# Optimization experiments

Measured on AMD Instinct MI355X. Metric: run time of the kernel, lower is better.

The kernel has to match this reference:

```python
import jax, jax.numpy as jnp
import numpy as np

B, H, W = 4, 64, 1024
h, w = 32, 512
K = 16
C = 64
EPS = 1e-5


def setup_inputs() -> dict:
    key = jax.random.key(0)
    ks = jax.random.split(key, 8)
    n_sampled = h * w
    xyz_proj = jax.random.normal(ks[0], (B, H, W, 3), dtype=jnp.float32)
    points_proj = jax.random.normal(ks[1], (B, H, W, C), dtype=jnp.float32)
    xyz_sampled_proj = jax.random.normal(ks[2], (B, h, w, 3), dtype=jnp.float32)
    # Precomputed neighbor selection (stand-in for fused_conv_random_k, which is
    # a non-differentiable custom CUDA op producing detached indices + mask).
    neighbor_idx = jax.random.randint(ks[3], (B, n_sampled * K), 0, H * W, dtype=jnp.int32)
    valid_mask = (jax.random.uniform(ks[4], (B, n_sampled, K, 1)) > 0.1).astype(jnp.float32)
    # 1x1 conv MLP params (torch Conv2d weight (out,in,1,1) stored here as (in,out))
    def mk(k, cin, cout):
        kw, = jax.random.split(k, 1)
        wgt = jax.random.normal(kw, (cin, cout), dtype=jnp.float32) * (1.0 / np.sqrt(cin))
        return wgt
    w0 = mk(ks[5], 3 + C, 64)
    w1 = mk(ks[6], 64, 64)
    w2 = mk(ks[7], 64, 128)
    z = lambda c: jnp.zeros((c,), jnp.float32)
    o = lambda c: jnp.ones((c,), jnp.float32)
    return dict(
        xyz_proj=xyz_proj, points_proj=points_proj, xyz_sampled_proj=xyz_sampled_proj,
        neighbor_idx=neighbor_idx, valid_mask=valid_mask,
        w0=w0, b0=z(64), g0=o(64), be0=z(64), m0=z(64), v0=o(64),
        w1=w1, b1=z(64), g1=o(64), be1=z(64), m1=z(64), v1=o(64),
        w2=w2, b2=z(128), g2=o(128), be2=z(128), m2=z(128), v2=o(128),
    )


def _conv_bn_relu(x, wgt, b, g, be, m, v):
    # 1x1 conv == matmul over channel dim; BN in eval mode with running stats.
    y = jnp.einsum('bnkc,co->bnko', x, wgt) + b
    y = g * (y - m) * jax.lax.rsqrt(v + EPS) + be
    return jax.nn.relu(y)


def reference(xyz_proj, points_proj, xyz_sampled_proj, neighbor_idx, valid_mask,
              w0, b0, g0, be0, m0, v0,
              w1, b1, g1, be1, m1, v1,
              w2, b2, g2, be2, m2, v2):
    Bc = xyz_proj.shape[0]
    Cc = points_proj.shape[3]
    hh, ww = xyz_sampled_proj.shape[1], xyz_sampled_proj.shape[2]
    n_sampled = hh * ww
    xyz_bn3 = xyz_proj.reshape(Bc, -1, 3)          # (B, H*W, 3)
    points_bnc = points_proj.reshape(Bc, -1, Cc)   # (B, H*W, C)
    idx = neighbor_idx[..., None]                  # (B, n*K, 1)
    new_xyz_group = jnp.take_along_axis(xyz_bn3, idx, axis=1).reshape(Bc, n_sampled, K, 3)
    new_points_group = jnp.take_along_axis(points_bnc, idx, axis=1).reshape(Bc, n_sampled, K, Cc)
    new_xyz_group = new_xyz_group * valid_mask
    new_points_group = new_points_group * valid_mask
    new_xyz = xyz_sampled_proj.reshape(Bc, n_sampled, 1, 3)
    xyz_diff = new_xyz_group - new_xyz             # broadcast over K
    feat = jnp.concatenate([xyz_diff, new_points_group], axis=-1)  # (B, n, K, 3+C)
    feat = _conv_bn_relu(feat, w0, b0, g0, be0, m0, v0)
    feat = _conv_bn_relu(feat, w1, b1, g1, be1, m1, v1)
    feat = _conv_bn_relu(feat, w2, b2, g2, be2, m2, v2)
    points_down_sample = jnp.max(feat, axis=2)     # (B, n, 128) max-pool over K
    points_down_sample_proj = points_down_sample.reshape(Bc, hh, ww, -1)
    return points_down_sample, points_down_sample_proj
```

## Files before the change

### kernel.cpp

```cpp
#include <hip/hip_runtime.h>
#include <hip/hip_bf16.h>


#define HW_      65536
#define NPT_     16384
#define OUTHALF_ 8388608
#define F0S_     104
#define XS_      72
#define EPS_     1e-5f

typedef _Float16 h8    __attribute__((ext_vector_type(8)));
typedef float    f32x4 __attribute__((ext_vector_type(4)));
typedef unsigned short u16x8 __attribute__((ext_vector_type(8)));

__device__ __forceinline__ float bf2f(unsigned short u) {
    union { unsigned int i; float f; } x; x.i = ((unsigned int)u) << 16; return x.f;
}
__device__ __forceinline__ unsigned short f2bf(float f) {
    union { float f; unsigned int i; } x; x.f = f;
    unsigned int r = x.i + 0x7fffu + ((x.i >> 16) & 1u);
    return (unsigned short)(r >> 16);
}

template<bool F32>
__device__ __forceinline__ float ldp(const void* p, int i) {
    if (F32) return ((const float*)p)[i];
    return bf2f(((const unsigned short*)p)[i]);
}

template<bool F32>
__global__ __launch_bounds__(256, 2) void pnsa_kernel(
    const void* __restrict__ xyz,
    const void* __restrict__ pts,
    const void* __restrict__ xyzs,
    const int*  __restrict__ nidx,
    const void* __restrict__ vmask,
    const void* __restrict__ w0, const void* __restrict__ b0,
    const void* __restrict__ g0, const void* __restrict__ be0,
    const void* __restrict__ m0, const void* __restrict__ v0,
    const void* __restrict__ w1, const void* __restrict__ b1,
    const void* __restrict__ g1, const void* __restrict__ be1,
    const void* __restrict__ m1, const void* __restrict__ v1,
    const void* __restrict__ w2, const void* __restrict__ b2,
    const void* __restrict__ g2, const void* __restrict__ be2,
    const void* __restrict__ m2, const void* __restrict__ v2,
    void*       __restrict__ out)
{
    const unsigned int probe = *(const unsigned int*)v0;
    const bool isf32 = (probe == 0x3F800000u);
    if (isf32 != F32) return;

    __shared__ __align__(16) unsigned short ldsF0[4][16 * F0S_];
    __shared__ __align__(16) unsigned short ldsX1[4][16 * XS_];
    __shared__ __align__(16) unsigned short ldsX2[4][16 * XS_];

    const int tid  = threadIdx.x;
    const int wave = tid >> 6;
    const int lane = tid & 63;
    const int l15  = lane & 15;
    const int quad = lane >> 4;

    unsigned short* F0 = &ldsF0[wave][0];
    unsigned short* X1 = &ldsX1[wave][0];
    unsigned short* X2 = &ldsX2[wave][0];

    for (int i = lane; i < 16 * F0S_; i += 64) F0[i] = 0;

    h8    b0f[4][3], b1f[4][2], b2f[8][2];
    float t0r[4], t1r[4], t2r[8];

#pragma unroll
    for (int nt = 0; nt < 4; ++nt) {
        const int ch = nt * 16 + l15;
        const float s = ldp<F32>(g0, ch) * rsqrtf(ldp<F32>(v0, ch) + EPS_);
        t0r[nt] = (ldp<F32>(b0, ch) - ldp<F32>(m0, ch)) * s + ldp<F32>(be0, ch);
#pragma unroll
        for (int kk = 0; kk < 3; ++kk) {
            h8 f;
#pragma unroll
            for (int j = 0; j < 8; ++j) {
                const int k = kk * 32 + quad * 8 + j;
                float wv = 0.f;
                if (k < 64)      wv = ldp<F32>(w0, (3 + k) * 64 + ch);
                else if (k < 67) wv = ldp<F32>(w0, (k - 64) * 64 + ch);
                f[j] = (_Float16)(wv * s);
            }
            b0f[nt][kk] = f;
        }
    }
#pragma unroll
    for (int nt = 0; nt < 4; ++nt) {
        const int ch = nt * 16 + l15;
        const float s = ldp<F32>(g1, ch) * rsqrtf(ldp<F32>(v1, ch) + EPS_);
        t1r[nt] = (ldp<F32>(b1, ch) - ldp<F32>(m1, ch)) * s + ldp<F32>(be1, ch);
#pragma unroll
        for (int kk = 0; kk < 2; ++kk) {
            h8 f;
#pragma unroll
            for (int j = 0; j < 8; ++j)
                f[j] = (_Float16)(ldp<F32>(w1, (kk * 32 + quad * 8 + j) * 64 + ch) * s);
            b1f[nt][kk] = f;
        }
    }
#pragma unroll
    for (int nt = 0; nt < 8; ++nt) {
        const int ch = nt * 16 + l15;
        const float s = ldp<F32>(g2, ch) * rsqrtf(ldp<F32>(v2, ch) + EPS_);
        t2r[nt] = (ldp<F32>(b2, ch) - ldp<F32>(m2, ch)) * s + ldp<F32>(be2, ch);
#pragma unroll
        for (int kk = 0; kk < 2; ++kk) {
            h8 f;
#pragma unroll
            for (int j = 0; j < 8; ++j)
                f[j] = (_Float16)(ldp<F32>(w2, (kk * 32 + quad * 8 + j) * 128 + ch) * s);
            b2f[nt][kk] = f;
        }
    }

    const int kn  = lane >> 2;
    const int sub = lane & 3;

    for (int grp = blockIdx.x; grp < NPT_; grp += gridDim.x) {
        const int p  = (grp << 2) + wave;
        const int b  = p >> 14;
        const int np = p & (NPT_ - 1);

        const int   nb = nidx[((size_t)b << 18) + ((size_t)np << 4) + kn];
        const float mk = ldp<F32>(vmask, (p << 4) + kn);
        const size_t rowidx = (size_t)((b << 16) + nb);

        h8 lo, hi;
        if (F32) {
            const float* prow = (const float*)pts + (rowidx << 6) + sub * 16;
#pragma unroll
            for (int q = 0; q < 2; ++q) {
                f32x4 v = *(const f32x4*)(prow + q * 4);
#pragma unroll
                for (int j = 0; j < 4; ++j) lo[q * 4 + j] = (_Float16)v[j];
            }
#pragma unroll
            for (int q = 0; q < 2; ++q) {
                f32x4 v = *(const f32x4*)(prow + 8 + q * 4);
#pragma unroll
                for (int j = 0; j < 4; ++j) hi[q * 4 + j] = (_Float16)v[j];
            }
        } else {
            const unsigned short* prow = (const unsigned short*)pts + (rowidx << 6) + sub * 16;
            u16x8 p0 = *(const u16x8*)(prow);
            u16x8 p1 = *(const u16x8*)(prow + 8);
#pragma unroll
            for (int j = 0; j < 8; ++j) { lo[j] = (_Float16)bf2f(p0[j]); hi[j] = (_Float16)bf2f(p1[j]); }
        }
        if (mk == 0.0f) { lo = (h8)(_Float16)0.0f; hi = (h8)(_Float16)0.0f; }
        *(h8*)(F0 + kn * F0S_ + sub * 16)     = lo;
        *(h8*)(F0 + kn * F0S_ + sub * 16 + 8) = hi;

        if (sub == 0) {
            float xg0, xg1, xg2, xs0, xs1, xs2;
            if (F32) {
                const float* xg = (const float*)xyz  + rowidx * 3;
                const float* xs = (const float*)xyzs + (size_t)p * 3;
                xg0 = xg[0]; xg1 = xg[1]; xg2 = xg[2];
                xs0 = xs[0]; xs1 = xs[1]; xs2 = xs[2];
            } else {
                const unsigned short* xg = (const unsigned short*)xyz  + rowidx * 3;
                const unsigned short* xs = (const unsigned short*)xyzs + (size_t)p * 3;
                xg0 = bf2f(xg[0]); xg1 = bf2f(xg[1]); xg2 = bf2f(xg[2]);
                xs0 = bf2f(xs[0]); xs1 = bf2f(xs[1]); xs2 = bf2f(xs[2]);
            }
            _Float16 xd[4];
            xd[0] = (_Float16)(xg0 * mk - xs0);
            xd[1] = (_Float16)(xg1 * mk - xs1);
            xd[2] = (_Float16)(xg2 * mk - xs2);
            xd[3] = (_Float16)0.0f;
            *(unsigned long long*)(F0 + kn * F0S_ + 64) = *(unsigned long long*)xd;
        }

        h8 a[3];

#pragma unroll
        for (int kk = 0; kk < 3; ++kk)
            a[kk] = *(const h8*)(F0 + l15 * F0S_ + kk * 32 + quad * 8);
#pragma unroll
        for (int nt = 0; nt < 4; ++nt) {
            f32x4 acc = {0.f, 0.f, 0.f, 0.f};
#pragma unroll
            for (int kk = 0; kk < 3; ++kk)
                acc = __builtin_amdgcn_mfma_f32_16x16x32_f16(a[kk], b0f[nt][kk], acc, 0, 0, 0);
#pragma unroll
            for (int r = 0; r < 4; ++r) {
                const _Float16 hv = (_Float16)fmaxf(acc[r] + t0r[nt], 0.f);
                X1[(quad * 4 + r) * XS_ + nt * 16 + l15] = __builtin_bit_cast(unsigned short, hv);
            }
        }

#pragma unroll
        for (int kk = 0; kk < 2; ++kk)
            a[kk] = *(const h8*)(X1 + l15 * XS_ + kk * 32 + quad * 8);
#pragma unroll
        for (int nt = 0; nt < 4; ++nt) {
            f32x4 acc = {0.f, 0.f, 0.f, 0.f};
#pragma unroll
            for (int kk = 0; kk < 2; ++kk)
                acc = __builtin_amdgcn_mfma_f32_16x16x32_f16(a[kk], b1f[nt][kk], acc, 0, 0, 0);
#pragma unroll
            for (int r = 0; r < 4; ++r) {
                const _Float16 hv = (_Float16)fmaxf(acc[r] + t1r[nt], 0.f);
                X2[(quad * 4 + r) * XS_ + nt * 16 + l15] = __builtin_bit_cast(unsigned short, hv);
            }
        }

#pragma unroll
        for (int kk = 0; kk < 2; ++kk)
            a[kk] = *(const h8*)(X2 + l15 * XS_ + kk * 32 + quad * 8);
#pragma unroll
        for (int nt = 0; nt < 8; ++nt) {
            f32x4 acc = {0.f, 0.f, 0.f, 0.f};
#pragma unroll
            for (int kk = 0; kk < 2; ++kk)
                acc = __builtin_amdgcn_mfma_f32_16x16x32_f16(a[kk], b2f[nt][kk], acc, 0, 0, 0);
            float rm = 0.f;
#pragma unroll
            for (int r = 0; r < 4; ++r) rm = fmaxf(rm, acc[r] + t2r[nt]);
            rm = fmaxf(rm, __shfl_xor(rm, 16, 64));
            rm = fmaxf(rm, __shfl_xor(rm, 32, 64));
            if (quad == 0) {
                const int oidx = (p << 7) + nt * 16 + l15;
                if (F32) {
                    ((float*)out)[oidx]            = rm;
                    ((float*)out)[OUTHALF_ + oidx] = rm;
                } else {
                    const unsigned short ob = f2bf(rm);
                    ((unsigned short*)out)[oidx]            = ob;
                    ((unsigned short*)out)[OUTHALF_ + oidx] = ob;
                }
            }
        }
    }
}

extern "C" void kernel_launch(void* const* d_in, const int* in_sizes, int n_in,
                              void* d_out, int out_size, void* d_ws, size_t ws_size,
                              hipStream_t stream) {
    const void* xyz   = d_in[0];
    const void* pts   = d_in[1];
    const void* xyzs  = d_in[2];
    const int*  nidx  = (const int*)d_in[3];
    const void* vmask = d_in[4];
    const void *w0 = d_in[5],  *b0 = d_in[6],  *g0 = d_in[7],  *be0 = d_in[8],  *m0 = d_in[9],  *v0 = d_in[10];
    const void *w1 = d_in[11], *b1 = d_in[12], *g1 = d_in[13], *be1 = d_in[14], *m1 = d_in[15], *v1 = d_in[16];
    const void *w2 = d_in[17], *b2 = d_in[18], *g2 = d_in[19], *be2 = d_in[20], *m2 = d_in[21], *v2 = d_in[22];

    hipLaunchKernelGGL(pnsa_kernel<true>, dim3(1024), dim3(256), 0, stream,
                       xyz, pts, xyzs, nidx, vmask,
                       w0, b0, g0, be0, m0, v0,
                       w1, b1, g1, be1, m1, v1,
                       w2, b2, g2, be2, m2, v2, d_out);
    hipLaunchKernelGGL(pnsa_kernel<false>, dim3(1024), dim3(256), 0, stream,
                       xyz, pts, xyzs, nidx, vmask,
                       w0, b0, g0, be0, m0, v0,
                       w1, b1, g1, be1, m1, v1,
                       w2, b2, g2, be2, m2, v2, d_out);
}
```

Measured before the change: 264.9 us.

## Pre-convert points to fp16, load MFMA operands directly, prefetch next iteration

Drops the dual bf16/fp32 template launch and keeps only the fp32 path. When workspace allows, a separate kernel first converts points to fp16, halving the bytes of the random row gather. The gathered rows now load straight into MFMA A-fragments instead of going through an LDS staging buffer. A software pipeline prefetches neighbor indices and row data one or two iterations ahead, and outputs are written as coalesced full-wave stores. The cost is an extra full pass over the points tensor, which must be recovered by the cheaper gather.

Result: faster. 231.7 us (-12.5%).

```diff
diff --git a/kernel.cpp b/kernel.cpp
--- a/kernel.cpp
+++ b/kernel.cpp
@@ -1,56 +1,47 @@
 #include <hip/hip_runtime.h>
-#include <hip/hip_bf16.h>
 
 
 #define HW_      65536
 #define NPT_     16384
 #define OUTHALF_ 8388608
-#define F0S_     104
 #define XS_      72
 #define EPS_     1e-5f
+#define GRID_    1024
+#define NIT_     (NPT_ / GRID_)
 
 typedef _Float16 h8    __attribute__((ext_vector_type(8)));
 typedef float    f32x4 __attribute__((ext_vector_type(4)));
-typedef unsigned short u16x8 __attribute__((ext_vector_type(8)));
-
-__device__ __forceinline__ float bf2f(unsigned short u) {
-    union { unsigned int i; float f; } x; x.i = ((unsigned int)u) << 16; return x.f;
+
+__global__ __launch_bounds__(256) void cvt_pts_kernel(
+    const float* __restrict__ src, _Float16* __restrict__ dst)
+{
+    const size_t i = ((size_t)blockIdx.x * 256 + threadIdx.x) * 8;
+    f32x4 a = *(const f32x4*)(src + i);
+    f32x4 b = *(const f32x4*)(src + i + 4);
+    h8 o;
+#pragma unroll
+    for (int j = 0; j < 4; ++j) { o[j] = (_Float16)a[j]; o[4 + j] = (_Float16)b[j]; }
+    *(h8*)(dst + i) = o;
 }
-__device__ __forceinline__ unsigned short f2bf(float f) {
-    union { float f; unsigned int i; } x; x.f = f;
-    unsigned int r = x.i + 0x7fffu + ((x.i >> 16) & 1u);
-    return (unsigned short)(r >> 16);
-}
-
-template<bool F32>
-__device__ __forceinline__ float ldp(const void* p, int i) {
-    if (F32) return ((const float*)p)[i];
-    return bf2f(((const unsigned short*)p)[i]);
-}
-
-template<bool F32>
-__global__ __launch_bounds__(256, 2) void pnsa_kernel(
-    const void* __restrict__ xyz,
-    const void* __restrict__ pts,
-    const void* __restrict__ xyzs,
-    const int*  __restrict__ nidx,
-    const void* __restrict__ vmask,
-    const void* __restrict__ w0, const void* __restrict__ b0,
-    const void* __restrict__ g0, const void* __restrict__ be0,
-    const void* __restrict__ m0, const void* __restrict__ v0,
-    const void* __restrict__ w1, const void* __restrict__ b1,
-    const void* __restrict__ g1, const void* __restrict__ be1,
-    const void* __restrict__ m1, const void* __restrict__ v1,
-    const void* __restrict__ w2, const void* __restrict__ b2,
-    const void* __restrict__ g2, const void* __restrict__ be2,
-    const void* __restrict__ m2, const void* __restrict__ v2,
-    void*       __restrict__ out)
+
+template<bool PRE>
+__global__ __launch_bounds__(256, 2) void pnsa_main(
+    const float* __restrict__ xyz,
+    const void*  __restrict__ ptsv,
+    const float* __restrict__ xyzs,
+    const int*   __restrict__ nidx,
+    const float* __restrict__ vmask,
+    const float* __restrict__ w0, const float* __restrict__ b0,
+    const float* __restrict__ g0, const float* __restrict__ be0,
+    const float* __restrict__ m0, const float* __restrict__ v0,
+    const float* __restrict__ w1, const float* __restrict__ b1,
+    const float* __restrict__ g1, const float* __restrict__ be1,
+    const float* __restrict__ m1, const float* __restrict__ v1,
+    const float* __restrict__ w2, const float* __restrict__ b2,
+    const float* __restrict__ g2, const float* __restrict__ be2,
+    const float* __restrict__ m2, const float* __restrict__ v2,
+    float*       __restrict__ out)
 {
-    const unsigned int probe = *(const unsigned int*)v0;
-    const bool isf32 = (probe == 0x3F800000u);
-    if (isf32 != F32) return;
-
-    __shared__ __align__(16) unsigned short ldsF0[4][16 * F0S_];
     __shared__ __align__(16) unsigned short ldsX1[4][16 * XS_];
     __shared__ __align__(16) unsigned short ldsX2[4][16 * XS_];
 
@@ -60,20 +51,17 @@
     const int l15  = lane & 15;
     const int quad = lane >> 4;
 
-    unsigned short* F0 = &ldsF0[wave][0];
     unsigned short* X1 = &ldsX1[wave][0];
     unsigned short* X2 = &ldsX2[wave][0];
 
-    for (int i = lane; i < 16 * F0S_; i += 64) F0[i] = 0;
-
     h8    b0f[4][3], b1f[4][2], b2f[8][2];
     float t0r[4], t1r[4], t2r[8];
 
 #pragma unroll
     for (int nt = 0; nt < 4; ++nt) {
         const int ch = nt * 16 + l15;
-        const float s = ldp<F32>(g0, ch) * rsqrtf(ldp<F32>(v0, ch) + EPS_);
-        t0r[nt] = (ldp<F32>(b0, ch) - ldp<F32>(m0, ch)) * s + ldp<F32>(be0, ch);
+        const float s = g0[ch] * rsqrtf(v0[ch] + EPS_);
+        t0r[nt] = (b0[ch] - m0[ch]) * s + be0[ch];
 #pragma unroll
         for (int kk = 0; kk < 3; ++kk) {
             h8 f;
@@ -81,8 +69,8 @@
             for (int j = 0; j < 8; ++j) {
                 const int k = kk * 32 + quad * 8 + j;
                 float wv = 0.f;
-                if (k < 64)      wv = ldp<F32>(w0, (3 + k) * 64 + ch);
-                else if (k < 67) wv = ldp<F32>(w0, (k - 64) * 64 + ch);
+                if (k < 64)      wv = w0[(3 + k) * 64 + ch];
+                else if (k < 67) wv = w0[(k - 64) * 64 + ch];
                 f[j] = (_Float16)(wv * s);
             }
             b0f[nt][kk] = f;
@@ -91,102 +79,103 @@
 #pragma unroll
     for (int nt = 0; nt < 4; ++nt) {
         const int ch = nt * 16 + l15;
-        const float s = ldp<F32>(g1, ch) * rsqrtf(ldp<F32>(v1, ch) + EPS_);
-        t1r[nt] = (ldp<F32>(b1, ch) - ldp<F32>(m1, ch)) * s + ldp<F32>(be1, ch);
+        const float s = g1[ch] * rsqrtf(v1[ch] + EPS_);
+        t1r[nt] = (b1[ch] - m1[ch]) * s + be1[ch];
 #pragma unroll
         for (int kk = 0; kk < 2; ++kk) {
             h8 f;
 #pragma unroll
             for (int j = 0; j < 8; ++j)
-                f[j] = (_Float16)(ldp<F32>(w1, (kk * 32 + quad * 8 + j) * 64 + ch) * s);
+                f[j] = (_Float16)(w1[(kk * 32 + quad * 8 + j) * 64 + ch] * s);
             b1f[nt][kk] = f;
         }
     }
 #pragma unroll
     for (int nt = 0; nt < 8; ++nt) {
         const int ch = nt * 16 + l15;
-        const float s = ldp<F32>(g2, ch) * rsqrtf(ldp<F32>(v2, ch) + EPS_);
-        t2r[nt] = (ldp<F32>(b2, ch) - ldp<F32>(m2, ch)) * s + ldp<F32>(be2, ch);
+        const float s = g2[ch] * rsqrtf(v2[ch] + EPS_);
+        t2r[nt] = (b2[ch] - m2[ch]) * s + be2[ch];
 #pragma unroll
         for (int kk = 0; kk < 2; ++kk) {
             h8 f;
 #pragma unroll
             for (int j = 0; j < 8; ++j)
-                f[j] = (_Float16)(ldp<F32>(w2, (kk * 32 + quad * 8 + j) * 128 + ch) * s);
+                f[j] = (_Float16)(w2[(kk * 32 + quad * 8 + j) * 128 + ch] * s);
             b2f[nt][kk] = f;
         }
     }
 
-    const int kn  = lane >> 2;
-    const int sub = lane & 3;
-
-    for (int grp = blockIdx.x; grp < NPT_; grp += gridDim.x) {
-        const int p  = (grp << 2) + wave;
-        const int b  = p >> 14;
-        const int np = p & (NPT_ - 1);
-
-        const int   nb = nidx[((size_t)b << 18) + ((size_t)np << 4) + kn];
-        const float mk = ldp<F32>(vmask, (p << 4) + kn);
-        const size_t rowidx = (size_t)((b << 16) + nb);
-
-        h8 lo, hi;
-        if (F32) {
-            const float* prow = (const float*)pts + (rowidx << 6) + sub * 16;
-#pragma unroll
-            for (int q = 0; q < 2; ++q) {
-                f32x4 v = *(const f32x4*)(prow + q * 4);
-#pragma unroll
-                for (int j = 0; j < 4; ++j) lo[q * 4 + j] = (_Float16)v[j];
-            }
-#pragma unroll
-            for (int q = 0; q < 2; ++q) {
-                f32x4 v = *(const f32x4*)(prow + 8 + q * 4);
-#pragma unroll
-                for (int j = 0; j < 4; ++j) hi[q * 4 + j] = (_Float16)v[j];
-            }
+    auto issue_pts = [&](int p_, int nb_, h8& q0, h8& q1,
+                         float& xga, float& xgb, float& xgc) {
+        const size_t row = (size_t)(((p_ >> 14) << 16) + nb_);
+        if constexpr (PRE) {
+            const _Float16* pw = (const _Float16*)ptsv + (row << 6);
+            q0 = *(const h8*)(pw + quad * 8);
+            q1 = *(const h8*)(pw + 32 + quad * 8);
+        }
+        const float* xgp = xyz + row * 3;
+        xga = xgp[0]; xgb = xgp[1]; xgc = xgp[2];
+    };
+    auto issue_aux = [&](int p_, float& xsa, float& xsb, float& xsc, float& mk) {
+        mk = vmask[(p_ << 4) + l15];
+        const float* xsp = xyzs + (size_t)p_ * 3;
+        xsa = xsp[0]; xsb = xsp[1]; xsc = xsp[2];
+    };
+
+    const int g = blockIdx.x;
+    const int p0 = (g << 2) + wave;
+    int nbc = nidx[(p0 << 4) + l15];
+    h8 q0c, q1c;
+    float xg0c, xg1c, xg2c, xs0c, xs1c, xs2c, mkc;
+    issue_pts(p0, nbc, q0c, q1c, xg0c, xg1c, xg2c);
+    issue_aux(p0, xs0c, xs1c, xs2c, mkc);
+    const int g1i = (NIT_ > 1) ? g + GRID_ : g;
+    int nbn = nidx[((((g1i << 2) + wave)) << 4) + l15];
+
+    for (int it = 0; it < NIT_; ++it) {
+        const int gcur = g + it * GRID_;
+        const int pcur = (gcur << 2) + wave;
+        const int gn   = (it + 1 < NIT_) ? gcur + GRID_ : gcur;
+        const int pn   = (gn << 2) + wave;
+        const int gn2  = (it + 2 < NIT_) ? gcur + 2 * GRID_ : gn;
+        const int pn2  = (gn2 << 2) + wave;
+
+        h8 q0n, q1n;
+        float xg0n, xg1n, xg2n, xs0n, xs1n, xs2n, mkn;
+        issue_pts(pn, nbn, q0n, q1n, xg0n, xg1n, xg2n);
+        issue_aux(pn, xs0n, xs1n, xs2n, mkn);
+        const int nbn2 = nidx[(pn2 << 4) + l15];
+
+        h8 a0, a1, a2;
+        if constexpr (PRE) {
+            a0 = q0c; a1 = q1c;
         } else {
-            const unsigned short* prow = (const unsigned short*)pts + (rowidx << 6) + sub * 16;
-            u16x8 p0 = *(const u16x8*)(prow);
-            u16x8 p1 = *(const u16x8*)(prow + 8);
-#pragma unroll
-            for (int j = 0; j < 8; ++j) { lo[j] = (_Float16)bf2f(p0[j]); hi[j] = (_Float16)bf2f(p1[j]); }
-        }
-        if (mk == 0.0f) { lo = (h8)(_Float16)0.0f; hi = (h8)(_Float16)0.0f; }
-        *(h8*)(F0 + kn * F0S_ + sub * 16)     = lo;
-        *(h8*)(F0 + kn * F0S_ + sub * 16 + 8) = hi;
-
-        if (sub == 0) {
-            float xg0, xg1, xg2, xs0, xs1, xs2;
-            if (F32) {
-                const float* xg = (const float*)xyz  + rowidx * 3;
-                const float* xs = (const float*)xyzs + (size_t)p * 3;
-                xg0 = xg[0]; xg1 = xg[1]; xg2 = xg[2];
-                xs0 = xs[0]; xs1 = xs[1]; xs2 = xs[2];
-            } else {
-                const unsigned short* xg = (const unsigned short*)xyz  + rowidx * 3;
-                const unsigned short* xs = (const unsigned short*)xyzs + (size_t)p * 3;
-                xg0 = bf2f(xg[0]); xg1 = bf2f(xg[1]); xg2 = bf2f(xg[2]);
-                xs0 = bf2f(xs[0]); xs1 = bf2f(xs[1]); xs2 = bf2f(xs[2]);
-            }
-            _Float16 xd[4];
-            xd[0] = (_Float16)(xg0 * mk - xs0);
-            xd[1] = (_Float16)(xg1 * mk - xs1);
-            xd[2] = (_Float16)(xg2 * mk - xs2);
-            xd[3] = (_Float16)0.0f;
-            *(unsigned long long*)(F0 + kn * F0S_ + 64) = *(unsigned long long*)xd;
-        }
-
-        h8 a[3];
-
-#pragma unroll
-        for (int kk = 0; kk < 3; ++kk)
-            a[kk] = *(const h8*)(F0 + l15 * F0S_ + kk * 32 + quad * 8);
+            const size_t row = (size_t)(((pcur >> 14) << 16) + nbc);
+            const float* pw = (const float*)ptsv + (row << 6);
+            f32x4 r0 = *(const f32x4*)(pw + quad * 8);
+            f32x4 r1 = *(const f32x4*)(pw + quad * 8 + 4);
+            f32x4 r2 = *(const f32x4*)(pw + 32 + quad * 8);
+            f32x4 r3 = *(const f32x4*)(pw + 32 + quad * 8 + 4);
+#pragma unroll
+            for (int j = 0; j < 4; ++j) {
+                a0[j] = (_Float16)r0[j]; a0[4 + j] = (_Float16)r1[j];
+                a1[j] = (_Float16)r2[j]; a1[4 + j] = (_Float16)r3[j];
+            }
+        }
+        if (mkc == 0.0f) { a0 = (h8)(_Float16)0.f; a1 = (h8)(_Float16)0.f; }
+        a2 = (h8)(_Float16)0.f;
+        if (quad == 0) {
+            a2[0] = (_Float16)(xg0c * mkc - xs0c);
+            a2[1] = (_Float16)(xg1c * mkc - xs1c);
+            a2[2] = (_Float16)(xg2c * mkc - xs2c);
+        }
+
 #pragma unroll
         for (int nt = 0; nt < 4; ++nt) {
             f32x4 acc = {0.f, 0.f, 0.f, 0.f};
-#pragma unroll
-            for (int kk = 0; kk < 3; ++kk)
-                acc = __builtin_amdgcn_mfma_f32_16x16x32_f16(a[kk], b0f[nt][kk], acc, 0, 0, 0);
+            acc = __builtin_amdgcn_mfma_f32_16x16x32_f16(a0, b0f[nt][0], acc, 0, 0, 0);
+            acc = __builtin_amdgcn_mfma_f32_16x16x32_f16(a1, b0f[nt][1], acc, 0, 0, 0);
+            acc = __builtin_amdgcn_mfma_f32_16x16x32_f16(a2, b0f[nt][2], acc, 0, 0, 0);
 #pragma unroll
             for (int r = 0; r < 4; ++r) {
                 const _Float16 hv = (_Float16)fmaxf(acc[r] + t0r[nt], 0.f);
@@ -194,15 +183,13 @@
             }
         }
 
-#pragma unroll
-        for (int kk = 0; kk < 2; ++kk)
-            a[kk] = *(const h8*)(X1 + l15 * XS_ + kk * 32 + quad * 8);
+        h8 x0 = *(const h8*)(X1 + l15 * XS_ + quad * 8);
+        h8 x1 = *(const h8*)(X1 + l15 * XS_ + 32 + quad * 8);
 #pragma unroll
         for (int nt = 0; nt < 4; ++nt) {
             f32x4 acc = {0.f, 0.f, 0.f, 0.f};
-#pragma unroll
-            for (int kk = 0; kk < 2; ++kk)
-                acc = __builtin_amdgcn_mfma_f32_16x16x32_f16(a[kk], b1f[nt][kk], acc, 0, 0, 0);
+            acc = __builtin_amdgcn_mfma_f32_16x16x32_f16(x0, b1f[nt][0], acc, 0, 0, 0);
+            acc = __builtin_amdgcn_mfma_f32_16x16x32_f16(x1, b1f[nt][1], acc, 0, 0, 0);
 #pragma unroll
             for (int r = 0; r < 4; ++r) {
                 const _Float16 hv = (_Float16)fmaxf(acc[r] + t1r[nt], 0.f);
@@ -210,55 +197,72 @@
             }
         }
 
-#pragma unroll
-        for (int kk = 0; kk < 2; ++kk)
-            a[kk] = *(const h8*)(X2 + l15 * XS_ + kk * 32 + quad * 8);
+        h8 y0 = *(const h8*)(X2 + l15 * XS_ + quad * 8);
+        h8 y1 = *(const h8*)(X2 + l15 * XS_ + 32 + quad * 8);
+        float rm[8];
 #pragma unroll
         for (int nt = 0; nt < 8; ++nt) {
             f32x4 acc = {0.f, 0.f, 0.f, 0.f};
-#pragma unroll
-            for (int kk = 0; kk < 2; ++kk)
-                acc = __builtin_amdgcn_mfma_f32_16x16x32_f16(a[kk], b2f[nt][kk], acc, 0, 0, 0);
-            float rm = 0.f;
-#pragma unroll
-            for (int r = 0; r < 4; ++r) rm = fmaxf(rm, acc[r] + t2r[nt]);
-            rm = fmaxf(rm, __shfl_xor(rm, 16, 64));
-            rm = fmaxf(rm, __shfl_xor(rm, 32, 64));
-            if (quad == 0) {
-                const int oidx = (p << 7) + nt * 16 + l15;
-                if (F32) {
-                    ((float*)out)[oidx]            = rm;
-                    ((float*)out)[OUTHALF_ + oidx] = rm;
-                } else {
-                    const unsigned short ob = f2bf(rm);
-                    ((unsigned short*)out)[oidx]            = ob;
-                    ((unsigned short*)out)[OUTHALF_ + oidx] = ob;
-                }
-            }
-        }
+            acc = __builtin_amdgcn_mfma_f32_16x16x32_f16(y0, b2f[nt][0], acc, 0, 0, 0);
+            acc = __builtin_amdgcn_mfma_f32_16x16x32_f16(y1, b2f[nt][1], acc, 0, 0, 0);
+            float v = 0.f;
+#pragma unroll
+            for (int r = 0; r < 4; ++r) v = fmaxf(v, acc[r] + t2r[nt]);
+            v = fmaxf(v, __shfl_xor(v, 16, 64));
+            v = fmaxf(v, __shfl_xor(v, 32, 64));
+            rm[nt] = v;
+        }
+        float* ob = out + ((size_t)pcur << 7);
+#pragma unroll
+        for (int ntg = 0; ntg < 2; ++ntg) {
+            const float s01 = (quad == 0) ? rm[ntg * 4 + 0] : rm[ntg * 4 + 1];
+            const float s23 = (quad == 2) ? rm[ntg * 4 + 2] : rm[ntg * 4 + 3];
+            const float vv  = (quad < 2) ? s01 : s23;
+            ob[ntg * 64 + lane]            = vv;
+            ob[OUTHALF_ + ntg * 64 + lane] = vv;
+        }
+
+        nbc = nbn; nbn = nbn2;
+        q0c = q0n; q1c = q1n;
+        xg0c = xg0n; xg1c = xg1n; xg2c = xg2n;
+        xs0c = xs0n; xs1c = xs1n; xs2c = xs2n;
+        mkc = mkn;
     }
 }
 
 extern "C" void kernel_launch(void* const* d_in, const int* in_sizes, int n_in,
                               void* d_out, int out_size, void* d_ws, size_t ws_size,
                               hipStream_t stream) {
-    const void* xyz   = d_in[0];
-    const void* pts   = d_in[1];
-    const void* xyzs  = d_in[2];
-    const int*  nidx  = (const int*)d_in[3];
-    const void* vmask = d_in[4];
-    const void *w0 = d_in[5],  *b0 = d_in[6],  *g0 = d_in[7],  *be0 = d_in[8],  *m0 = d_in[9],  *v0 = d_in[10];
-    const void *w1 = d_in[11], *b1 = d_in[12], *g1 = d_in[13], *be1 = d_in[14], *m1 = d_in[15], *v1 = d_in[16];
-    const void *w2 = d_in[17], *b2 = d_in[18], *g2 = d_in[19], *be2 = d_in[20], *m2 = d_in[21], *v2 = d_in[22];
-
-    hipLaunchKernelGGL(pnsa_kernel<true>, dim3(1024), dim3(256), 0, stream,
-                       xyz, pts, xyzs, nidx, vmask,
-                       w0, b0, g0, be0, m0, v0,
-                       w1, b1, g1, be1, m1, v1,
-                       w2, b2, g2, be2, m2, v2, d_out);
-    hipLaunchKernelGGL(pnsa_kernel<false>, dim3(1024), dim3(256), 0, stream,
-                       xyz, pts, xyzs, nidx, vmask,
-                       w0, b0, g0, be0, m0, v0,
-                       w1, b1, g1, be1, m1, v1,
-                       w2, b2, g2, be2, m2, v2, d_out);
+    const float* xyz   = (const float*)d_in[0];
+    const float* pts   = (const float*)d_in[1];
+    const float* xyzs  = (const float*)d_in[2];
+    const int*   nidx  = (const int*)d_in[3];
+    const float* vmask = (const float*)d_in[4];
+    const float *w0 = (const float*)d_in[5],  *b0 = (const float*)d_in[6],
+                *g0 = (const float*)d_in[7],  *be0 = (const float*)d_in[8],
+                *m0 = (const float*)d_in[9],  *v0 = (const float*)d_in[10];
+    const float *w1 = (const float*)d_in[11], *b1 = (const float*)d_in[12],
+                *g1 = (const float*)d_in[13], *be1 = (const float*)d_in[14],
+                *m1 = (const float*)d_in[15], *v1 = (const float*)d_in[16];
+    const float *w2 = (const float*)d_in[17], *b2 = (const float*)d_in[18],
+                *g2 = (const float*)d_in[19], *be2 = (const float*)d_in[20],
+                *m2 = (const float*)d_in[21], *v2 = (const float*)d_in[22];
+    float* outp = (float*)d_out;
+
+    const size_t PTS_ELEMS = 16777216ull;
+    if (ws_size >= PTS_ELEMS * sizeof(_Float16)) {
+        _Float16* ptsh = (_Float16*)d_ws;
+        cvt_pts_kernel<<<dim3(8192), dim3(256), 0, stream>>>(pts, ptsh);
+        pnsa_main<true><<<dim3(GRID_), dim3(256), 0, stream>>>(
+            xyz, (const void*)ptsh, xyzs, nidx, vmask,
+            w0, b0, g0, be0, m0, v0,
+            w1, b1, g1, be1, m1, v1,
+            w2, b2, g2, be2, m2, v2, outp);
+    } else {
+        pnsa_main<false><<<dim3(GRID_), dim3(256), 0, stream>>>(
+            xyz, (const void*)pts, xyzs, nidx, vmask,
+            w0, b0, g0, be0, m0, v0,
+            w1, b1, g1, be1, m1, v1,
+            w2, b2, g2, be2, m2, v2, outp);
+    }
 }
```
